# Kernel optimization log

Hardware: AMD Instinct MI355X
Metric: run time of the kernel (lower is better)

Reference implementation:

```python
import jax, jax.numpy as jnp
import numpy as np

N, E = 20000, 320000
D, DW, DS, NCLS = 512, 300, 16, 13


def setup_inputs() -> dict:
    key = jax.random.key(0)
    ks = jax.random.split(key, 24)
    g = lambda k, s, sc=0.02: (jax.random.normal(k, s, dtype=jnp.float32) * sc)
    inp = {
        'n_f': jax.random.normal(ks[0], (N, D), dtype=jnp.float32),
        'word2vec': jax.random.normal(ks[1], (N, DW), dtype=jnp.float32),
        's_f': jax.random.normal(ks[2], (E, DS), dtype=jnp.float32),
        'src': jax.random.randint(ks[3], (E,), 0, N, dtype=jnp.int32),
        'dst': jax.random.randint(ks[4], (E,), 0, N, dtype=jnp.int32),
        # edge MLPs: G_E_L_S=[2*D+DS, D], G_E_L_S2=[2*DW, D]
        'W_e': g(ks[5], (2 * D + DS, D)), 'b_e': jnp.zeros((D,), jnp.float32),
        'W_el': g(ks[6], (2 * DW, D)), 'b_el': jnp.zeros((D,), jnp.float32),
        # attention MLPs: G_A_L_S=[D,1], G_A_L_S2=[D,1]
        'W_a': g(ks[7], (D, 1)), 'b_a': jnp.zeros((1,), jnp.float32),
        'W_al': g(ks[8], (D, 1)), 'b_al': jnp.zeros((1,), jnp.float32),
        # node MLPs: G_N_L_S=[2*D, D], G_N_L_S2=[2*DW, DW]
        'W_n': g(ks[9], (2 * D, D)), 'b_n': jnp.zeros((D,), jnp.float32),
        'W_nl': g(ks[10], (2 * DW, DW)), 'b_nl': jnp.zeros((DW,), jnp.float32),
        # edge readout: G_ER_L_S=[2*D+2*DW+DS, D, 13], acts ['ReLU','Identity']
        'W_r1': g(ks[11], (2 * D + 2 * DW + DS, D)), 'b_r1': jnp.zeros((D,), jnp.float32),
        'W_r2': g(ks[12], (D, NCLS)), 'b_r2': jnp.zeros((NCLS,), jnp.float32),
    }
    return inp


def _segment_softmax(logits, seg, num_segments):
    m = jax.ops.segment_max(logits, seg, num_segments=num_segments)
    m = jnp.where(jnp.isfinite(m), m, 0.0)
    e = jnp.exp(logits - m[seg])
    s = jax.ops.segment_sum(e, seg, num_segments=num_segments)
    return e / (s[seg] + 1e-9)


def _forward(n_f, word2vec, s_f, W_e, b_e, W_el, b_el, W_a, b_a, W_al, b_al,
             W_n, b_n, W_nl, b_nl, W_r1, b_r1, W_r2, b_r2, src, dst):
    n = n_f.shape[0]
    relu = jax.nn.relu
    # H_H_EdgeApplyModule: e_f = ReLU(MLP([src n_f, s_f, dst n_f]))
    feat = jnp.concatenate([n_f[src], s_f, n_f[dst]], axis=1)            # [E, 2D+DS]
    e_f = relu(feat @ W_e + b_e)                                         # [E, D]
    feat_lang = jnp.concatenate([word2vec[src], word2vec[dst]], axis=1)  # [E, 2DW]
    e_f_lang = relu(feat_lang @ W_el + b_el)                             # [E, D]
    # E_AttentionModule1: LeakyReLU(0.2) attention logits per edge
    a = jax.nn.leaky_relu(e_f @ W_a + b_a, 0.2)[:, 0]
    a_l = jax.nn.leaky_relu(e_f_lang @ W_al + b_al, 0.2)[:, 0]
    # edge-softmax over incoming edges of each destination node
    alpha = _segment_softmax(a, dst, n)
    alpha_l = _segment_softmax(a_l, dst, n)
    # attention-weighted aggregation (scatter-add per dst node)
    z = jax.ops.segment_sum(alpha[:, None] * e_f, dst, num_segments=n)            # [N, D]
    z_l = jax.ops.segment_sum(alpha_l[:, None] * word2vec[src], dst, num_segments=n)  # [N, DW]
    # H_NodeApplyModule: node update with ReLU MLPs
    n_new = relu(jnp.concatenate([n_f, z], axis=1) @ W_n + b_n)          # [N, D]
    w_new = relu(jnp.concatenate([word2vec, z_l], axis=1) @ W_nl + b_nl) # [N, DW]
    # edge readout (G_ER): [src n_f, src w2v, s_f, dst w2v, dst n_f] -> ReLU -> Identity
    r = jnp.concatenate([n_new[src], w_new[src], s_f, w_new[dst], n_new[dst]], axis=1)
    h = relu(r @ W_r1 + b_r1)
    return h @ W_r2 + b_r2                                               # [E, 13]


def reference(n_f, word2vec, s_f, src, dst, W_e, b_e, W_el, b_el, W_a, b_a,
              W_al, b_al, W_n, b_n, W_nl, b_nl, W_r1, b_r1, W_r2, b_r2):
    return _forward(n_f, word2vec, s_f, W_e, b_e, W_el, b_el, W_a, b_a, W_al, b_al,
                    W_n, b_n, W_nl, b_nl, W_r1, b_r1, W_r2, b_r2, src, dst)
```

## Files before the change

### kernel.cpp

```cpp
#include <hip/hip_runtime.h>

typedef unsigned short u16;
typedef unsigned int u32;
typedef __bf16 bf16x8 __attribute__((ext_vector_type(8)));
typedef float f32x4 __attribute__((ext_vector_type(4)));

#define ND 512
#define DWR 300
#define DWP 320
#define NCLS 13

__device__ __forceinline__ float bf2f(u16 u) { return __uint_as_float(((u32)u) << 16); }
__device__ __forceinline__ u16 f2bf(float f) {
    u32 u = __float_as_uint(f);
    u32 r = (u + 0x7FFFu + ((u >> 16) & 1u)) >> 16;
    return (u16)r;
}
__device__ __forceinline__ void ub8(float4 r, float* v) {
    union { float4 f; u16 u[8]; } U; U.f = r;
#pragma unroll
    for (int k = 0; k < 8; ++k) v[k] = bf2f(U.u[k]);
}
__device__ __forceinline__ void ld8f(const u16* p, float* v) { ub8(*(const float4*)p, v); }
__device__ __forceinline__ void ld16(const float* p, float* s) {
    const float4* sp = (const float4*)p;
    float4 s0 = sp[0], s1 = sp[1], s2 = sp[2], s3 = sp[3];
    s[0]=s0.x; s[1]=s0.y; s[2]=s0.z; s[3]=s0.w; s[4]=s1.x; s[5]=s1.y; s[6]=s1.z; s[7]=s1.w;
    s[8]=s2.x; s[9]=s2.y; s[10]=s2.z; s[11]=s2.w; s[12]=s3.x; s[13]=s3.y; s[14]=s3.z; s[15]=s3.w;
}

struct GSeg { const u16* base; const int* idx; int stride; int width; };
struct GSegs { GSeg s[5]; };
struct TSeg { int src_begin; int wreal; int wpad; };
struct TSegs { TSeg t[5]; };

template<int RELU>
__global__ __launch_bounds__(256) void gemm_k(
    int M, int Nout, GSegs segs,
    const u16* __restrict__ BT, int ldb,
    const float* __restrict__ bias, int bias_n,
    u16* __restrict__ outb, int ldo)
{
    __shared__ __align__(16) u16 As[128 * 40];
    __shared__ __align__(16) u16 Bs[128 * 40];
    const int tid = threadIdx.x;

    const int gx = gridDim.x, gy = gridDim.y;
    const int g0 = blockIdx.x + gx * blockIdx.y;
    int xt, yt;
    {
        const int fullg = gx >> 3;
        const int gsz = 8 * gy;
        if (g0 < fullg * gsz) {
            const int grp = g0 / gsz, w = g0 % gsz;
            xt = grp * 8 + (w & 7); yt = w >> 3;
        } else {
            const int remx = gx - fullg * 8;
            const int t = g0 - fullg * gsz;
            xt = fullg * 8 + t % remx; yt = t / remx;
        }
    }
    const int m0 = xt * 128, n0 = yt * 128;

    const int row = tid >> 1, half = tid & 1;
    int mrow = m0 + row; if (mrow >= M) mrow = M - 1;
    const int lane = tid & 63, wid = tid >> 6;
    const int wr = (wid >> 1) * 64, wc = (wid & 1) * 64;
    const int lr = lane & 15, lg = lane >> 4;

    f32x4 acc[4][4];
    for (int fm = 0; fm < 4; fm++)
        for (int fn = 0; fn < 4; fn++)
            acc[fm][fn] = f32x4{0.f, 0.f, 0.f, 0.f};

    const u16* brow = BT + (size_t)(n0 + row) * ldb + half * 16;

    auto do_step = [&](const u16* ga_, const u16* gb_) {
        float4 a0 = *(const float4*)ga_;
        float4 a1 = *(const float4*)(ga_ + 8);
        float4 b0 = *(const float4*)gb_;
        float4 b1 = *(const float4*)(gb_ + 8);
        __syncthreads();
        *(float4*)&As[row * 40 + half * 16]     = a0;
        *(float4*)&As[row * 40 + half * 16 + 8] = a1;
        *(float4*)&Bs[row * 40 + half * 16]     = b0;
        *(float4*)&Bs[row * 40 + half * 16 + 8] = b1;
        __syncthreads();
        bf16x8 af[4], bfv[4];
#pragma unroll
        for (int f = 0; f < 4; f++) {
            af[f]  = *(const bf16x8*)&As[(wr + f * 16 + lr) * 40 + lg * 8];
            bfv[f] = *(const bf16x8*)&Bs[(wc + f * 16 + lr) * 40 + lg * 8];
        }
#pragma unroll
        for (int fm = 0; fm < 4; fm++)
#pragma unroll
            for (int fn = 0; fn < 4; fn++)
                acc[fm][fn] = __builtin_amdgcn_mfma_f32_16x16x32_bf16(af[fm], bfv[fn], acc[fm][fn], 0, 0, 0);
    };

    int k0 = 0;
#pragma unroll
    for (int sI = 0; sI < 5; sI++) {
        const GSeg S = segs.s[sI];
        if (S.width > 0) {
            const int ridx = S.idx ? S.idx[mrow] : mrow;
            const u16* abase = S.base + (size_t)ridx * S.stride + half * 16;
            for (int kk = 0; kk < S.width; kk += 32) {
                do_step(abase + kk, brow + k0 + kk);
            }
            k0 += S.width;
        }
    }

#pragma unroll
    for (int fm = 0; fm < 4; fm++) {
#pragma unroll
        for (int i = 0; i < 4; i++) {
            const int grow = m0 + wr + fm * 16 + lg * 4 + i;
            const bool rok = grow < M;
#pragma unroll
            for (int fn = 0; fn < 4; fn++) {
                const int col = n0 + wc + fn * 16 + lr;
                float v = acc[fm][fn][i];
                v += (col < bias_n) ? bias[col] : 0.f;
                if (RELU) v = fmaxf(v, 0.f);
                if (rok && col < Nout) outb[(size_t)grow * ldo + col] = f2bf(v);
            }
        }
    }
}

__global__ __launch_bounds__(256) void pass1_k(
    const u16* __restrict__ Q, const u16* __restrict__ Lq,
    const float* __restrict__ s_f, const float* __restrict__ wmid,
    const int* __restrict__ psrc, const int* __restrict__ perm, const int* __restrict__ offs,
    const float* __restrict__ W_a, const float* __restrict__ W_al,
    const float* __restrict__ b_e, const float* __restrict__ b_el,
    const float* __restrict__ b_a, const float* __restrict__ b_al,
    float* __restrict__ aA, float* __restrict__ aL, int N, int E)
{
    __shared__ __align__(16) u16 wmids[16 * 512];
    const int tid = threadIdx.x;
    for (int i = tid; i < 16 * 512; i += 256) wmids[i] = f2bf(wmid[i]);
    __syncthreads();
    const int node = blockIdx.x * 4 + (tid >> 6);
    if (node >= N) return;
    const int lane = tid & 63;
    const int col0 = lane * 8;
    const int e0 = offs[node];
    const int e1 = (node + 1 < N) ? offs[node + 1] : E;
    if (e0 >= e1) return;

    float q2b[8], l2b[8], wa[8], wal[8], t[8];
    ld8f(Q + (size_t)node * 1024 + 512 + col0, q2b);
    ld8f(Lq + (size_t)node * 1024 + 512 + col0, l2b);
#pragma unroll
    for (int k = 0; k < 8; ++k) {
        q2b[k] += b_e[col0 + k]; l2b[k] += b_el[col0 + k];
        wa[k] = W_a[col0 + k];   wal[k] = W_al[col0 + k];
    }
    const float ba = b_a[0], bal = b_al[0];

    int ps0 = psrc[e0], pe0 = perm[e0];
    float4 rq0 = *(const float4*)(Q + (size_t)ps0 * 1024 + col0);
    float4 rl0 = *(const float4*)(Lq + (size_t)ps0 * 1024 + col0);
    int ps1 = ps0, pe1 = pe0;
    if (e0 + 1 < e1) { ps1 = psrc[e0 + 1]; pe1 = perm[e0 + 1]; }

    for (int e = e0; e < e1; ++e) {
        float4 rq1 = rq0, rl1 = rl0;
        if (e + 1 < e1) {
            rq1 = *(const float4*)(Q + (size_t)ps1 * 1024 + col0);
            rl1 = *(const float4*)(Lq + (size_t)ps1 * 1024 + col0);
        }
        int ps2 = ps1, pe2 = pe1;
        if (e + 2 < e1) { ps2 = psrc[e + 2]; pe2 = perm[e + 2]; }

        float sf[16];
        ld16(s_f + (size_t)pe0 * 16, sf);
        float v[8];
        ub8(rq0, t);
#pragma unroll
        for (int k = 0; k < 8; ++k) v[k] = t[k] + q2b[k];
#pragma unroll
        for (int j = 0; j < 16; ++j) {
            union { float4 f; u16 u[8]; } W;
            W.f = *(const float4*)&wmids[j * 512 + col0];
#pragma unroll
            for (int k = 0; k < 8; ++k) v[k] = fmaf(sf[j], bf2f(W.u[k]), v[k]);
        }
        float ap = 0.f, al = 0.f;
#pragma unroll
        for (int k = 0; k < 8; ++k) ap = fmaf(fmaxf(v[k], 0.f), wa[k], ap);
        ub8(rl0, t);
#pragma unroll
        for (int k = 0; k < 8; ++k) al = fmaf(fmaxf(t[k] + l2b[k], 0.f), wal[k], al);
#pragma unroll
        for (int off = 32; off >= 1; off >>= 1) {
            ap += __shfl_xor(ap, off, 64);
            al += __shfl_xor(al, off, 64);
        }
        if (lane == 0) {
            float x = ap + ba;  aA[e] = x > 0.f ? x : 0.2f * x;
            float y = al + bal; aL[e] = y > 0.f ? y : 0.2f * y;
        }
        rq0 = rq1; rl0 = rl1; ps0 = ps1; pe0 = pe1; ps1 = ps2; pe1 = pe2;
    }
}

__global__ __launch_bounds__(256) void softmax_k(
    float* __restrict__ a, float* __restrict__ al,
    const int* __restrict__ offs, int N, int E)
{
    const int node = blockIdx.x * 4 + (threadIdx.x >> 6);
    if (node >= N) return;
    const int lane = threadIdx.x & 63;
    const int e0 = offs[node];
    const int e1 = (node + 1 < N) ? offs[node + 1] : E;
    if (e0 >= e1) return;
    float m = -3.4e38f, ml = -3.4e38f;
    for (int e = e0 + lane; e < e1; e += 64) { m = fmaxf(m, a[e]); ml = fmaxf(ml, al[e]); }
#pragma unroll
    for (int off = 32; off >= 1; off >>= 1) {
        m  = fmaxf(m,  __shfl_xor(m,  off, 64));
        ml = fmaxf(ml, __shfl_xor(ml, off, 64));
    }
    float s = 0.f, sl = 0.f;
    for (int e = e0 + lane; e < e1; e += 64) {
        float v = expf(a[e] - m);   a[e] = v;  s += v;
        float w = expf(al[e] - ml); al[e] = w; sl += w;
    }
#pragma unroll
    for (int off = 32; off >= 1; off >>= 1) {
        s  += __shfl_xor(s,  off, 64);
        sl += __shfl_xor(sl, off, 64);
    }
    const float rs = 1.f / (s + 1e-9f), rsl = 1.f / (sl + 1e-9f);
    for (int e = e0 + lane; e < e1; e += 64) { a[e] *= rs; al[e] *= rsl; }
}

__global__ __launch_bounds__(256) void passz_k(
    const u16* __restrict__ Q, const u16* __restrict__ wv_bf,
    const float* __restrict__ s_f, const float* __restrict__ wmid,
    const int* __restrict__ psrc, const int* __restrict__ perm, const int* __restrict__ offs,
    const float* __restrict__ alpha, const float* __restrict__ alphal,
    const float* __restrict__ b_e,
    u16* __restrict__ z_bf, u16* __restrict__ zl_bf, int N, int E)
{
    __shared__ __align__(16) u16 wmids[16 * 512];
    const int tid = threadIdx.x;
    for (int i = tid; i < 16 * 512; i += 256) wmids[i] = f2bf(wmid[i]);
    __syncthreads();
    const int node = blockIdx.x * 4 + (tid >> 6);
    if (node >= N) return;
    const int lane = tid & 63;
    const int col0 = lane * 8;
    const int colw = (lane < 40) ? col0 : 0;
    const int e0 = offs[node];
    const int e1 = (node + 1 < N) ? offs[node + 1] : E;

    float q2b[8], accz[8], accl[8], t[8];
    ld8f(Q + (size_t)node * 1024 + 512 + col0, q2b);
#pragma unroll
    for (int k = 0; k < 8; ++k) { q2b[k] += b_e[col0 + k]; accz[k] = 0.f; accl[k] = 0.f; }

    if (e0 < e1) {
        int ps0 = psrc[e0], pe0 = perm[e0];
        float4 rq0 = *(const float4*)(Q + (size_t)ps0 * 1024 + col0);
        float4 rw0 = *(const float4*)(wv_bf + (size_t)ps0 * DWP + colw);
        int ps1 = ps0, pe1 = pe0;
        if (e0 + 1 < e1) { ps1 = psrc[e0 + 1]; pe1 = perm[e0 + 1]; }

        for (int e = e0; e < e1; ++e) {
            float4 rq1 = rq0, rw1 = rw0;
            if (e + 1 < e1) {
                rq1 = *(const float4*)(Q + (size_t)ps1 * 1024 + col0);
                rw1 = *(const float4*)(wv_bf + (size_t)ps1 * DWP + colw);
            }
            int ps2 = ps1, pe2 = pe1;
            if (e + 2 < e1) { ps2 = psrc[e + 2]; pe2 = perm[e + 2]; }

            const float alA = alpha[e], alL = alphal[e];
            float sf[16];
            ld16(s_f + (size_t)pe0 * 16, sf);
            float v[8];
            ub8(rq0, t);
#pragma unroll
            for (int k = 0; k < 8; ++k) v[k] = t[k] + q2b[k];
#pragma unroll
            for (int j = 0; j < 16; ++j) {
                union { float4 f; u16 u[8]; } W;
                W.f = *(const float4*)&wmids[j * 512 + col0];
#pragma unroll
                for (int k = 0; k < 8; ++k) v[k] = fmaf(sf[j], bf2f(W.u[k]), v[k]);
            }
#pragma unroll
            for (int k = 0; k < 8; ++k) accz[k] = fmaf(alA, fmaxf(v[k], 0.f), accz[k]);
            ub8(rw0, t);
#pragma unroll
            for (int k = 0; k < 8; ++k) accl[k] = fmaf(alL, t[k], accl[k]);

            rq0 = rq1; rw0 = rw1; ps0 = ps1; pe0 = pe1; ps1 = ps2; pe1 = pe2;
        }
    }
    union { float4 f; u16 u[8]; } O;
#pragma unroll
    for (int k = 0; k < 8; ++k) O.u[k] = f2bf(accz[k]);
    *(float4*)(z_bf + (size_t)node * 512 + col0) = O.f;
    if (lane < 40) {
#pragma unroll
        for (int k = 0; k < 8; ++k) O.u[k] = f2bf(accl[k]);
        *(float4*)(zl_bf + (size_t)node * DWP + col0) = O.f;
    }
}

__global__ __launch_bounds__(256) void pass3_k(
    const u16* __restrict__ P, const float* __restrict__ s_f, const float* __restrict__ wmid2,
    const int* __restrict__ psrc, const int* __restrict__ pdst, const int* __restrict__ perm,
    const float* __restrict__ b_r1, const float* __restrict__ w2, const float* __restrict__ b_r2,
    float* __restrict__ out, int E)
{
    __shared__ __align__(16) u16 As[128 * 40];
    __shared__ __align__(16) u16 wmid2s[16 * 520];
    __shared__ __align__(16) u16 w2Ts[16 * 520];
    __shared__ float sfs[16 * 128];
    __shared__ float br1s[512];

    const int tid = threadIdx.x;
    const int e0 = blockIdx.x * 128;

    for (int i = tid; i < 16 * 512; i += 256)
        wmid2s[(i >> 9) * 520 + (i & 511)] = f2bf(wmid2[i]);
    for (int i = tid; i < 16 * 512; i += 256) {
        const int c = i >> 9, k = i & 511;
        w2Ts[c * 520 + k] = f2bf((c < NCLS) ? w2[k * NCLS + c] : 0.f);
    }
    for (int i = tid; i < 512; i += 256) br1s[i] = b_r1[i];

    const int row = tid >> 1, half = tid & 1;
    const int er = e0 + row;
    const int erc = (er < E) ? er : E - 1;
    {
        const int pe = perm[erc];
        const int jh = half * 8;
        const float4* sp = (const float4*)(s_f + (size_t)pe * 16 + jh);
        float4 a = sp[0], b = sp[1];
        sfs[(jh + 0) * 128 + row] = a.x; sfs[(jh + 1) * 128 + row] = a.y;
        sfs[(jh + 2) * 128 + row] = a.z; sfs[(jh + 3) * 128 + row] = a.w;
        sfs[(jh + 4) * 128 + row] = b.x; sfs[(jh + 5) * 128 + row] = b.y;
        sfs[(jh + 6) * 128 + row] = b.z; sfs[(jh + 7) * 128 + row] = b.w;
    }

    const int ps = psrc[erc], pd = pdst[erc];
    const u16* p1base = P + (size_t)ps * 1024;
    const u16* p2base = P + (size_t)pd * 1024 + 512;

    const int lane = tid & 63, wid = tid >> 6;
    const int lr = lane & 15, lg = lane >> 4;
    f32x4 acc0 = f32x4{0.f, 0.f, 0.f, 0.f};
    f32x4 acc1 = f32x4{0.f, 0.f, 0.f, 0.f};

    __syncthreads();

    for (int ch = 0; ch < 16; ++ch) {
        const int k0 = ch * 32 + half * 16;
        float4 r1a = *(const float4*)(p1base + k0);
        float4 r1b = *(const float4*)(p1base + k0 + 8);
        float4 r2a = *(const float4*)(p2base + k0);
        float4 r2b = *(const float4*)(p2base + k0 + 8);
        float u[16], t1[8], t2[8];
        ub8(r1a, t1); ub8(r2a, t2);
#pragma unroll
        for (int k = 0; k < 8; ++k) u[k] = t1[k] + t2[k] + br1s[k0 + k];
        ub8(r1b, t1); ub8(r2b, t2);
#pragma unroll
        for (int k = 0; k < 8; ++k) u[8 + k] = t1[k] + t2[k] + br1s[k0 + 8 + k];
#pragma unroll
        for (int j = 0; j < 16; ++j) {
            const float sv = sfs[j * 128 + row];
            union { float4 f; u16 u[8]; } W1, W2;
            W1.f = *(const float4*)&wmid2s[j * 520 + k0];
            W2.f = *(const float4*)&wmid2s[j * 520 + k0 + 8];
#pragma unroll
            for (int k = 0; k < 8; ++k) {
                u[k]     = fmaf(sv, bf2f(W1.u[k]), u[k]);
                u[8 + k] = fmaf(sv, bf2f(W2.u[k]), u[8 + k]);
            }
        }
        union { float4 f; u16 u[8]; } Oa, Ob;
#pragma unroll
        for (int k = 0; k < 8; ++k) {
            Oa.u[k] = f2bf(fmaxf(u[k], 0.f));
            Ob.u[k] = f2bf(fmaxf(u[8 + k], 0.f));
        }
        __syncthreads();
        *(float4*)&As[row * 40 + half * 16]     = Oa.f;
        *(float4*)&As[row * 40 + half * 16 + 8] = Ob.f;
        __syncthreads();
        bf16x8 af0 = *(const bf16x8*)&As[(wid * 32 +      lr) * 40 + lg * 8];
        bf16x8 af1 = *(const bf16x8*)&As[(wid * 32 + 16 + lr) * 40 + lg * 8];
        bf16x8 bfv = *(const bf16x8*)&w2Ts[lr * 520 + ch * 32 + lg * 8];
        acc0 = __builtin_amdgcn_mfma_f32_16x16x32_bf16(af0, bfv, acc0, 0, 0, 0);
        acc1 = __builtin_amdgcn_mfma_f32_16x16x32_bf16(af1, bfv, acc1, 0, 0, 0);
    }

    if (lr < NCLS) {
        const float bc = b_r2[lr];
#pragma unroll
        for (int m = 0; m < 2; ++m) {
            const f32x4 a = m ? acc1 : acc0;
            const int rbase = e0 + wid * 32 + m * 16 + lg * 4;
#pragma unroll
            for (int i = 0; i < 4; ++i) {
                const int ei = rbase + i;
                if (ei < E) out[(size_t)perm[ei] * NCLS + lr] = a[i] + bc;
            }
        }
    }
}

__global__ __launch_bounds__(256) void cvt_bf(const float* __restrict__ src, u16* __restrict__ dst,
                                              int R, int Cs, int Cd)
{
    int id = blockIdx.x * 256 + threadIdx.x;
    if (id >= R * Cd) return;
    int r = id / Cd, c = id % Cd;
    float v = (c < Cs) ? src[(size_t)r * Cs + c] : 0.f;
    dst[id] = f2bf(v);
}

__global__ __launch_bounds__(256) void wtrans(const float* __restrict__ W, int Nw, int Nreal,
                                              int NrowsOut, int ldk, TSegs ts, int nseg,
                                              u16* __restrict__ WT)
{
    int id = blockIdx.x * 256 + threadIdx.x;
    if (id >= NrowsOut * ldk) return;
    int n = id / ldk, kp = id % ldk;
    float v = 0.f;
    if (n < Nreal) {
        int off = 0;
#pragma unroll
        for (int s = 0; s < 5; s++) {
            if (s < nseg) {
                int kl = kp - off;
                if (kl >= 0 && kl < ts.t[s].wpad) {
                    if (kl < ts.t[s].wreal) v = W[(size_t)(ts.t[s].src_begin + kl) * Nw + n];
                }
                off += ts.t[s].wpad;
            }
        }
    }
    WT[id] = f2bf(v);
}

__global__ __launch_bounds__(256) void hist_k(const int* __restrict__ dst, int* __restrict__ deg, int E)
{
    int id = blockIdx.x * 256 + threadIdx.x;
    if (id < E) atomicAdd(&deg[dst[id]], 1);
}

__global__ __launch_bounds__(1024) void scan_k(const int* __restrict__ deg,
                                               int* __restrict__ offs, int* __restrict__ cursor, int N)
{
    __shared__ int ps[1024];
    const int t = threadIdx.x;
    const int per = (N + 1023) >> 10;
    int s = 0;
    for (int j = 0; j < per; j++) { int idx = t * per + j; if (idx < N) s += deg[idx]; }
    ps[t] = s; __syncthreads();
    for (int o = 1; o < 1024; o <<= 1) {
        int v = (t >= o) ? ps[t - o] : 0; __syncthreads();
        ps[t] += v; __syncthreads();
    }
    int run = ps[t] - s;
    for (int j = 0; j < per; j++) {
        int idx = t * per + j;
        if (idx < N) { offs[idx] = run; cursor[idx] = run; run += deg[idx]; }
    }
}

__global__ __launch_bounds__(256) void scat_perm_k(const int* __restrict__ src, const int* __restrict__ dst,
                                                   int* __restrict__ cursor, int* __restrict__ perm,
                                                   int* __restrict__ psrc, int* __restrict__ pdst, int E)
{
    int id = blockIdx.x * 256 + threadIdx.x;
    if (id >= E) return;
    int d = dst[id];
    int pos = atomicAdd(&cursor[d], 1);
    perm[pos] = id; psrc[pos] = src[id]; pdst[pos] = d;
}

__global__ __launch_bounds__(256) void diag_fill(float* out, int n, float v)
{
    int id = blockIdx.x * 256 + threadIdx.x;
    if (id < n) out[id] = v;
}

extern "C" void kernel_launch(void* const* d_in, const int* in_sizes, int n_in,
                              void* d_out, int out_size, void* d_ws, size_t ws_size,
                              hipStream_t stream)
{
    const float* n_f  = (const float*)d_in[0];
    const float* w2v  = (const float*)d_in[1];
    const float* s_f  = (const float*)d_in[2];
    const int*   src  = (const int*)d_in[3];
    const int*   dst  = (const int*)d_in[4];
    const float* W_e  = (const float*)d_in[5];
    const float* b_e  = (const float*)d_in[6];
    const float* W_el = (const float*)d_in[7];
    const float* b_el = (const float*)d_in[8];
    const float* W_a  = (const float*)d_in[9];
    const float* b_a  = (const float*)d_in[10];
    const float* W_al = (const float*)d_in[11];
    const float* b_al = (const float*)d_in[12];
    const float* W_n  = (const float*)d_in[13];
    const float* b_n  = (const float*)d_in[14];
    const float* W_nl = (const float*)d_in[15];
    const float* b_nl = (const float*)d_in[16];
    const float* W_r1 = (const float*)d_in[17];
    const float* b_r1 = (const float*)d_in[18];
    const float* W_r2 = (const float*)d_in[19];
    const float* b_r2 = (const float*)d_in[20];

    const int N = in_sizes[0] / ND;
    const int E = in_sizes[3];
    float* out = (float*)d_out;

    auto g1 = [](long long n) { return dim3((unsigned)((n + 255) / 256)); };

    char* base = (char*)d_ws;
    size_t off = 0;
    auto alloc = [&](size_t bytes) -> void* {
        void* r = base + off;
        off += (bytes + 255) & ~(size_t)255;
        return r;
    };
    u16* nf_bf = (u16*)alloc((size_t)N * ND * 2);
    u16* wv_bf = (u16*)alloc((size_t)N * DWP * 2);
    u16* Q     = (u16*)alloc((size_t)N * 1024 * 2);
    u16* Lq    = (u16*)alloc((size_t)N * 1024 * 2);
    u16* Pt    = (u16*)alloc((size_t)N * 1024 * 2);
    u16* z_bf  = (u16*)alloc((size_t)N * ND * 2);
    u16* zl_bf = (u16*)alloc((size_t)N * DWP * 2);
    u16* nn_bf = (u16*)alloc((size_t)N * ND * 2);
    u16* wn_bf = (u16*)alloc((size_t)N * DWP * 2);
    u16* QT    = (u16*)alloc((size_t)1024 * 512 * 2);
    u16* LT    = (u16*)alloc((size_t)1024 * 320 * 2);
    u16* WnT   = (u16*)alloc((size_t)512 * 1024 * 2);
    u16* WnlT  = (u16*)alloc((size_t)384 * 640 * 2);
    u16* PrT   = (u16*)alloc((size_t)1024 * 832 * 2);
    float* aAs = (float*)alloc((size_t)E * 4);
    float* aLs = (float*)alloc((size_t)E * 4);
    int* deg    = (int*)alloc((size_t)N * 4);
    int* offs   = (int*)alloc((size_t)N * 4);
    int* cursor = (int*)alloc((size_t)N * 4);
    int* perm   = (int*)alloc((size_t)E * 4);
    int* psrc   = (int*)alloc((size_t)E * 4);
    int* pdst   = (int*)alloc((size_t)E * 4);

    if (off > ws_size) {
        diag_fill<<<g1(out_size), 256, 0, stream>>>(out, out_size, 2.0e6f);
        return;
    }

    hipMemsetAsync(deg, 0, (size_t)N * 4, stream);

    hist_k<<<g1(E), 256, 0, stream>>>(dst, deg, E);
    scan_k<<<dim3(1), 1024, 0, stream>>>(deg, offs, cursor, N);
    scat_perm_k<<<g1(E), 256, 0, stream>>>(src, dst, cursor, perm, psrc, pdst, E);

    cvt_bf<<<g1((long long)N * ND), 256, 0, stream>>>(n_f, nf_bf, N, ND, ND);
    cvt_bf<<<g1((long long)N * DWP), 256, 0, stream>>>(w2v, wv_bf, N, DWR, DWP);

    { TSegs t{}; t.t[0] = {0,512,512};
      wtrans<<<g1(512 * 512), 256, 0, stream>>>(W_e, 512, 512, 512, 512, t, 1, QT); }
    { TSegs t{}; t.t[0] = {528,512,512};
      wtrans<<<g1(512 * 512), 256, 0, stream>>>(W_e, 512, 512, 512, 512, t, 1, QT + 512 * 512); }
    { TSegs t{}; t.t[0] = {0,300,320};
      wtrans<<<g1(512 * 320), 256, 0, stream>>>(W_el, 512, 512, 512, 320, t, 1, LT); }
    { TSegs t{}; t.t[0] = {300,300,320};
      wtrans<<<g1(512 * 320), 256, 0, stream>>>(W_el, 512, 512, 512, 320, t, 1, LT + 512 * 320); }
    { TSegs t{}; t.t[0] = {0,512,512}; t.t[1] = {512,512,512};
      wtrans<<<g1(512 * 1024), 256, 0, stream>>>(W_n, 512, 512, 512, 1024, t, 2, WnT); }
    { TSegs t{}; t.t[0] = {0,300,320}; t.t[1] = {300,300,320};
      wtrans<<<g1(384 * 640), 256, 0, stream>>>(W_nl, 300, 300, 384, 640, t, 2, WnlT); }
    { TSegs t{}; t.t[0] = {0,512,512}; t.t[1] = {512,300,320};
      wtrans<<<g1(512 * 832), 256, 0, stream>>>(W_r1, 512, 512, 512, 832, t, 2, PrT); }
    { TSegs t{}; t.t[0] = {1128,512,512}; t.t[1] = {828,300,320};
      wtrans<<<g1(512 * 832), 256, 0, stream>>>(W_r1, 512, 512, 512, 832, t, 2, PrT + 512 * 832); }

    const int gmx = (N + 127) / 128;
    const dim3 gnode((N + 3) / 4);

    { GSegs s{}; s.s[0] = {nf_bf, nullptr, ND, 512};
      gemm_k<0><<<dim3(gmx, 8), 256, 0, stream>>>(N, 1024, s, QT, 512, nullptr, 0, Q, 1024); }
    { GSegs s{}; s.s[0] = {wv_bf, nullptr, DWP, 320};
      gemm_k<0><<<dim3(gmx, 8), 256, 0, stream>>>(N, 1024, s, LT, 320, nullptr, 0, Lq, 1024); }

    pass1_k<<<gnode, 256, 0, stream>>>(Q, Lq, s_f, W_e + 512 * 512, psrc, perm, offs,
                                       W_a, W_al, b_e, b_el, b_a, b_al, aAs, aLs, N, E);
    softmax_k<<<gnode, 256, 0, stream>>>(aAs, aLs, offs, N, E);

    passz_k<<<gnode, 256, 0, stream>>>(Q, wv_bf, s_f, W_e + 512 * 512, psrc, perm, offs,
                                       aAs, aLs, b_e, z_bf, zl_bf, N, E);

    { GSegs s{}; s.s[0] = {nf_bf, nullptr, ND, 512}; s.s[1] = {z_bf, nullptr, ND, 512};
      gemm_k<1><<<dim3(gmx, 4), 256, 0, stream>>>(N, 512, s, WnT, 1024, b_n, 512, nn_bf, 512); }
    { GSegs s{}; s.s[0] = {wv_bf, nullptr, DWP, 320}; s.s[1] = {zl_bf, nullptr, DWP, 320};
      gemm_k<1><<<dim3(gmx, 3), 256, 0, stream>>>(N, 320, s, WnlT, 640, b_nl, 300, wn_bf, DWP); }

    { GSegs s{}; s.s[0] = {nn_bf, nullptr, ND, 512}; s.s[1] = {wn_bf, nullptr, DWP, 320};
      gemm_k<0><<<dim3(gmx, 8), 256, 0, stream>>>(N, 1024, s, PrT, 832, nullptr, 0, Pt, 1024); }

    pass3_k<<<dim3((E + 127) / 128), 256, 0, stream>>>(Pt, s_f, W_r1 + 812 * 512,
                                                       psrc, pdst, perm, b_r1, W_r2, b_r2, out, E);

    hipError_t e = hipGetLastError();
    if (e != hipSuccess) {
        diag_fill<<<g1(out_size), 256, 0, stream>>>(out, out_size, 1.0e6f + (float)(int)e);
    }
}
```

Before: 1.056 ms.

## Restructure attention-logit pass as edge-tiled kernel with MFMA dot products

The attention logit pass previously ran one wavefront per destination node and walked that node's edges serially, doing shuffle reductions per edge. It now assigns 128 edges per block with two threads per edge, builds the ReLU'd hidden activations in bf16 shared memory, and reduces them against W_a/W_al with MFMA instructions. This removes the dependence on degree imbalance and the per-edge shuffle reductions. In exchange it re-reads the destination-side Q/Lq rows for every edge instead of once per node, and rounds the activations and attention weights to bf16.

```diff
diff --git a/kernel.cpp b/kernel.cpp
--- a/kernel.cpp
+++ b/kernel.cpp
@@ -134,78 +134,139 @@
 __global__ __launch_bounds__(256) void pass1_k(
     const u16* __restrict__ Q, const u16* __restrict__ Lq,
     const float* __restrict__ s_f, const float* __restrict__ wmid,
-    const int* __restrict__ psrc, const int* __restrict__ perm, const int* __restrict__ offs,
+    const int* __restrict__ psrc, const int* __restrict__ pdst, const int* __restrict__ perm,
     const float* __restrict__ W_a, const float* __restrict__ W_al,
     const float* __restrict__ b_e, const float* __restrict__ b_el,
     const float* __restrict__ b_a, const float* __restrict__ b_al,
-    float* __restrict__ aA, float* __restrict__ aL, int N, int E)
-{
-    __shared__ __align__(16) u16 wmids[16 * 512];
+    float* __restrict__ aA, float* __restrict__ aL, int E)
+{
+    __shared__ __align__(16) u16 wmids[16 * 520];
+    __shared__ __align__(16) u16 As_v[128 * 40];
+    __shared__ __align__(16) u16 As_l[128 * 40];
+    __shared__ float sfs[16 * 128];
+    __shared__ float bes[512], bels[512];
+    __shared__ __align__(16) u16 was[512], wals[512];
+
     const int tid = threadIdx.x;
-    for (int i = tid; i < 16 * 512; i += 256) wmids[i] = f2bf(wmid[i]);
+    const int e0 = blockIdx.x * 128;
+
+    for (int i = tid; i < 16 * 512; i += 256)
+        wmids[(i >> 9) * 520 + (i & 511)] = f2bf(wmid[i]);
+    for (int i = tid; i < 512; i += 256) {
+        bes[i] = b_e[i]; bels[i] = b_el[i];
+        was[i] = f2bf(W_a[i]); wals[i] = f2bf(W_al[i]);
+    }
+
+    const int row = tid >> 1, half = tid & 1;
+    const int er = e0 + row;
+    const int erc = (er < E) ? er : E - 1;
+    {
+        const int pe = perm[erc];
+        const int jh = half * 8;
+        const float4* sp = (const float4*)(s_f + (size_t)pe * 16 + jh);
+        float4 a = sp[0], b = sp[1];
+        sfs[(jh + 0) * 128 + row] = a.x; sfs[(jh + 1) * 128 + row] = a.y;
+        sfs[(jh + 2) * 128 + row] = a.z; sfs[(jh + 3) * 128 + row] = a.w;
+        sfs[(jh + 4) * 128 + row] = b.x; sfs[(jh + 5) * 128 + row] = b.y;
+        sfs[(jh + 6) * 128 + row] = b.z; sfs[(jh + 7) * 128 + row] = b.w;
+    }
+
+    const int ps = psrc[erc], pd = pdst[erc];
+    const u16* q1b = Q + (size_t)ps * 1024;
+    const u16* q2b = Q + (size_t)pd * 1024 + 512;
+    const u16* l1b = Lq + (size_t)ps * 1024;
+    const u16* l2b = Lq + (size_t)pd * 1024 + 512;
+
+    const int lane = tid & 63, wid = tid >> 6;
+    const int lr = lane & 15, lg = lane >> 4;
+    f32x4 accv[2], accl[2];
+    accv[0] = accv[1] = accl[0] = accl[1] = f32x4{0.f, 0.f, 0.f, 0.f};
+
+    union { bf16x8 v; float4 f; } BZ; BZ.f = float4{0.f, 0.f, 0.f, 0.f};
+
     __syncthreads();
-    const int node = blockIdx.x * 4 + (tid >> 6);
-    if (node >= N) return;
-    const int lane = tid & 63;
-    const int col0 = lane * 8;
-    const int e0 = offs[node];
-    const int e1 = (node + 1 < N) ? offs[node + 1] : E;
-    if (e0 >= e1) return;
-
-    float q2b[8], l2b[8], wa[8], wal[8], t[8];
-    ld8f(Q + (size_t)node * 1024 + 512 + col0, q2b);
-    ld8f(Lq + (size_t)node * 1024 + 512 + col0, l2b);
-#pragma unroll
-    for (int k = 0; k < 8; ++k) {
-        q2b[k] += b_e[col0 + k]; l2b[k] += b_el[col0 + k];
-        wa[k] = W_a[col0 + k];   wal[k] = W_al[col0 + k];
-    }
-    const float ba = b_a[0], bal = b_al[0];
-
-    int ps0 = psrc[e0], pe0 = perm[e0];
-    float4 rq0 = *(const float4*)(Q + (size_t)ps0 * 1024 + col0);
-    float4 rl0 = *(const float4*)(Lq + (size_t)ps0 * 1024 + col0);
-    int ps1 = ps0, pe1 = pe0;
-    if (e0 + 1 < e1) { ps1 = psrc[e0 + 1]; pe1 = perm[e0 + 1]; }
-
-    for (int e = e0; e < e1; ++e) {
-        float4 rq1 = rq0, rl1 = rl0;
-        if (e + 1 < e1) {
-            rq1 = *(const float4*)(Q + (size_t)ps1 * 1024 + col0);
-            rl1 = *(const float4*)(Lq + (size_t)ps1 * 1024 + col0);
-        }
-        int ps2 = ps1, pe2 = pe1;
-        if (e + 2 < e1) { ps2 = psrc[e + 2]; pe2 = perm[e + 2]; }
-
-        float sf[16];
-        ld16(s_f + (size_t)pe0 * 16, sf);
-        float v[8];
-        ub8(rq0, t);
-#pragma unroll
-        for (int k = 0; k < 8; ++k) v[k] = t[k] + q2b[k];
+
+    for (int ch = 0; ch < 16; ++ch) {
+        const int k0 = ch * 32 + half * 16;
+        float4 rq1a = *(const float4*)(q1b + k0);
+        float4 rq1b = *(const float4*)(q1b + k0 + 8);
+        float4 rq2a = *(const float4*)(q2b + k0);
+        float4 rq2b = *(const float4*)(q2b + k0 + 8);
+        float4 rl1a = *(const float4*)(l1b + k0);
+        float4 rl1b = *(const float4*)(l1b + k0 + 8);
+        float4 rl2a = *(const float4*)(l2b + k0);
+        float4 rl2b = *(const float4*)(l2b + k0 + 8);
+
+        float uv[16], ul[16], t1[8], t2[8];
+        ub8(rq1a, t1); ub8(rq2a, t2);
+#pragma unroll
+        for (int k = 0; k < 8; ++k) uv[k] = t1[k] + t2[k] + bes[k0 + k];
+        ub8(rq1b, t1); ub8(rq2b, t2);
+#pragma unroll
+        for (int k = 0; k < 8; ++k) uv[8 + k] = t1[k] + t2[k] + bes[k0 + 8 + k];
+        ub8(rl1a, t1); ub8(rl2a, t2);
+#pragma unroll
+        for (int k = 0; k < 8; ++k) ul[k] = t1[k] + t2[k] + bels[k0 + k];
+        ub8(rl1b, t1); ub8(rl2b, t2);
+#pragma unroll
+        for (int k = 0; k < 8; ++k) ul[8 + k] = t1[k] + t2[k] + bels[k0 + 8 + k];
+
 #pragma unroll
         for (int j = 0; j < 16; ++j) {
-            union { float4 f; u16 u[8]; } W;
-            W.f = *(const float4*)&wmids[j * 512 + col0];
-#pragma unroll
-            for (int k = 0; k < 8; ++k) v[k] = fmaf(sf[j], bf2f(W.u[k]), v[k]);
-        }
-        float ap = 0.f, al = 0.f;
-#pragma unroll
-        for (int k = 0; k < 8; ++k) ap = fmaf(fmaxf(v[k], 0.f), wa[k], ap);
-        ub8(rl0, t);
-#pragma unroll
-        for (int k = 0; k < 8; ++k) al = fmaf(fmaxf(t[k] + l2b[k], 0.f), wal[k], al);
-#pragma unroll
-        for (int off = 32; off >= 1; off >>= 1) {
-            ap += __shfl_xor(ap, off, 64);
-            al += __shfl_xor(al, off, 64);
-        }
-        if (lane == 0) {
-            float x = ap + ba;  aA[e] = x > 0.f ? x : 0.2f * x;
-            float y = al + bal; aL[e] = y > 0.f ? y : 0.2f * y;
-        }
-        rq0 = rq1; rl0 = rl1; ps0 = ps1; pe0 = pe1; ps1 = ps2; pe1 = pe2;
+            const float sv = sfs[j * 128 + row];
+            union { float4 f; u16 u[8]; } W1, W2;
+            W1.f = *(const float4*)&wmids[j * 520 + k0];
+            W2.f = *(const float4*)&wmids[j * 520 + k0 + 8];
+#pragma unroll
+            for (int k = 0; k < 8; ++k) {
+                uv[k]     = fmaf(sv, bf2f(W1.u[k]), uv[k]);
+                uv[8 + k] = fmaf(sv, bf2f(W2.u[k]), uv[8 + k]);
+            }
+        }
+        union { float4 f; u16 u[8]; } Va, Vb, La, Lb;
+#pragma unroll
+        for (int k = 0; k < 8; ++k) {
+            Va.u[k] = f2bf(fmaxf(uv[k], 0.f));
+            Vb.u[k] = f2bf(fmaxf(uv[8 + k], 0.f));
+            La.u[k] = f2bf(fmaxf(ul[k], 0.f));
+            Lb.u[k] = f2bf(fmaxf(ul[8 + k], 0.f));
+        }
+        __syncthreads();
+        *(float4*)&As_v[row * 40 + half * 16]     = Va.f;
+        *(float4*)&As_v[row * 40 + half * 16 + 8] = Vb.f;
+        *(float4*)&As_l[row * 40 + half * 16]     = La.f;
+        *(float4*)&As_l[row * 40 + half * 16 + 8] = Lb.f;
+        __syncthreads();
+
+        bf16x8 bv = BZ.v, bl = BZ.v;
+        if (lr == 0) {
+            bv = *(const bf16x8*)&was[ch * 32 + lg * 8];
+            bl = *(const bf16x8*)&wals[ch * 32 + lg * 8];
+        }
+#pragma unroll
+        for (int m = 0; m < 2; ++m) {
+            bf16x8 afv = *(const bf16x8*)&As_v[(wid * 32 + m * 16 + lr) * 40 + lg * 8];
+            bf16x8 afl = *(const bf16x8*)&As_l[(wid * 32 + m * 16 + lr) * 40 + lg * 8];
+            accv[m] = __builtin_amdgcn_mfma_f32_16x16x32_bf16(afv, bv, accv[m], 0, 0, 0);
+            accl[m] = __builtin_amdgcn_mfma_f32_16x16x32_bf16(afl, bl, accl[m], 0, 0, 0);
+        }
+    }
+
+    if (lr == 0) {
+        const float ba = b_a[0], bal = b_al[0];
+#pragma unroll
+        for (int m = 0; m < 2; ++m) {
+#pragma unroll
+            for (int i = 0; i < 4; ++i) {
+                const int e = e0 + wid * 32 + m * 16 + lg * 4 + i;
+                if (e < E) {
+                    float x = accv[m][i] + ba;
+                    aA[e] = x > 0.f ? x : 0.2f * x;
+                    float y = accl[m][i] + bal;
+                    aL[e] = y > 0.f ? y : 0.2f * y;
+                }
+            }
+        }
     }
 }
 
@@ -598,8 +659,9 @@
     { GSegs s{}; s.s[0] = {wv_bf, nullptr, DWP, 320};
       gemm_k<0><<<dim3(gmx, 8), 256, 0, stream>>>(N, 1024, s, LT, 320, nullptr, 0, Lq, 1024); }
 
-    pass1_k<<<gnode, 256, 0, stream>>>(Q, Lq, s_f, W_e + 512 * 512, psrc, perm, offs,
-                                       W_a, W_al, b_e, b_el, b_a, b_al, aAs, aLs, N, E);
+    pass1_k<<<dim3((E + 127) / 128), 256, 0, stream>>>(Q, Lq, s_f, W_e + 512 * 512,
+                                                       psrc, pdst, perm, W_a, W_al,
+                                                       b_e, b_el, b_a, b_al, aAs, aLs, E);
     softmax_k<<<gnode, 256, 0, stream>>>(aAs, aLs, offs, N, E);
 
     passz_k<<<gnode, 256, 0, stream>>>(Q, wv_bf, s_f, W_e + 512 * 512, psrc, perm, offs,
```

After: 1.009 ms. 1.05x faster.
